# Performance work log

Measured on AMD Instinct MI355X. Metric: run time of the kernel, lower is better.

The kernel has to match this reference:

```python
import jax, jax.numpy as jnp
import numpy as np
from jax import lax

STRIDE = 2
PAD = 2
K = 5

def conv_transpose3d(x, w, b):
    # x: (N, Cin, D, H, W); w: (Cin, Cout, kD, kH, kW) torch layout
    # Equivalent dense conv: flip kernel spatially, swap in/out, lhs-dilate by stride,
    # pad each side by (K - 1 - PAD).
    w_t = jnp.flip(w, axis=(2, 3, 4)).transpose(1, 0, 2, 3, 4)  # (Cout, Cin, kD, kH, kW)
    p = K - 1 - PAD  # = 2
    y = lax.conv_general_dilated(
        x, w_t,
        window_strides=(1, 1, 1),
        padding=[(p, p)] * 3,
        lhs_dilation=(STRIDE,) * 3,
        dimension_numbers=('NCDHW', 'OIDHW', 'NCDHW'))
    return y + b[None, :, None, None, None]

def maxpool3d(x, k):
    return lax.reduce_window(
        x, -jnp.inf, lax.max,
        window_dimensions=(1, 1, k, k, k),
        window_strides=(1, 1, k, k, k),
        padding='VALID')

def setup_inputs() -> dict:
    key = jax.random.key(0)
    k1, k2, k3 = jax.random.split(key, 3)
    x = jax.random.normal(k1, (16, 32, 16, 32, 32), dtype=jnp.float32)
    weight = jax.random.normal(k2, (32, 64, 5, 5, 5), dtype=jnp.float32) * 0.05
    bias = jax.random.normal(k3, (64,), dtype=jnp.float32) * 0.05
    return {"x": x, "weight": weight, "bias": bias}

def reference(x, weight, bias):
    y = conv_transpose3d(x, weight, bias)      # (16, 64, 31, 63, 63)
    y = maxpool3d(y, 2)                        # (16, 64, 15, 31, 31)
    y = maxpool3d(y, 3)                        # (16, 64, 5, 10, 10)
    return jnp.sum(y, axis=1, keepdims=True)   # (16, 1, 5, 10, 10)
```

## Files before the change

kernel.cpp:

```cpp
#include <hip/hip_runtime.h>

typedef short v8s __attribute__((ext_vector_type(8)));
typedef float v4f __attribute__((ext_vector_type(4)));

#define N_  16
#define CI_ 32
#define CO_ 64
#define DI  16
#define HI  32
#define WI  32
#define NEGINF (-__builtin_inff())

__device__ __forceinline__ unsigned short f2bf(float f) {
    unsigned int u = __float_as_uint(f);
    unsigned int r = (u + 0x7FFFu + ((u >> 16) & 1u)) >> 16;
    return (unsigned short)r;
}

__device__ __forceinline__ void gld16(const void* g, void* l) {
    __builtin_amdgcn_global_load_lds(
        (const __attribute__((address_space(1))) void*)g,
        (__attribute__((address_space(3))) void*)l, 16, 0, 0);
}

__constant__ int O64c[9] = {0, 55296, 92160, 129024, 153600, 190464, 215040, 239616, 256000};

__global__ void prep(const float* __restrict__ x, const float* __restrict__ w,
                     unsigned short* __restrict__ xp, unsigned short* __restrict__ wt,
                     float* __restrict__ out, int do_x) {
    if (blockIdx.x < 1088) {
        if (!do_x) return;
        __shared__ __align__(16) unsigned short tl[8192];
        const int bi = blockIdx.x;
        const int pd = bi % 17;
        const int cg = (bi / 17) & 3;
        const int n  = bi / 68;
        if (pd > 0) {
            const int c = threadIdx.x >> 5;
            const int ww = threadIdx.x & 31;
            const float* xc = x + (((size_t)(n * 32 + cg * 8 + c) * 16 + (pd - 1)) * 32) * 32;
            #pragma unroll
            for (int h = 0; h < 32; ++h)
                tl[(h * 32 + ww) * 8 + c] = f2bf(xc[h * 32 + ww]);
        }
        __syncthreads();
        unsigned short* xpo = xp + (size_t)bi * 8448;
        for (int o = threadIdx.x; o < 1056; o += 256) {
            int ph = o / 33, pw = o - ph * 33;
            v8s v;
            if (pd == 0 || ph == 0 || pw == 0) v = (v8s){0, 0, 0, 0, 0, 0, 0, 0};
            else v = *(const v8s*)&tl[((ph - 1) * 32 + pw - 1) * 8];
            *(v8s*)(xpo + o * 8) = v;
        }
    } else {
        if (blockIdx.x == 1088 && threadIdx.x < 64) {
            int tb = 1536 + threadIdx.x;
            int whalf = tb & 1, hj = (tb >> 1) % 10, dj = (tb / 20) % 5, n = tb / 100;
            float* o = out + (((size_t)(n * 5 + dj) * 10 + hj) * 10 + whalf * 5);
            #pragma unroll
            for (int j = 0; j < 5; ++j) o[j] = 0.f;
        }
        int u = (blockIdx.x - 1088) * 256 + threadIdx.x;
        if (u >= 256000) return;
        int r = 0;
        #pragma unroll
        for (int i = 1; i < 8; ++i) r += (u >= O64c[i]);
        const int rd = r >> 2, rh = (r >> 1) & 1, rw = r & 1;
        const int nh = rh ? 2 : 3, nw = rw ? 2 : 3;
        int t2 = u - O64c[r];
        int j   = t2 & 7;
        int l   = (t2 >> 3) & 15;
        int q   = (t2 >> 7) & 3;
        int nt  = (t2 >> 9) & 3;
        int tap = t2 >> 11;
        int co = nt * 16 + l;
        int ci = q * 8 + j;
        int jw = tap % nw;
        int jh = (tap / nw) % nh;
        int jd = tap / (nw * nh);
        int kd = rd + 2 * jd, kh = rh + 2 * jh, kw = rw + 2 * jw;
        wt[u] = f2bf(w[(ci * CO_ + co) * 125 + kd * 25 + kh * 5 + kw]);
    }
}

__device__ __forceinline__ void run_class_rt(
        const unsigned short* __restrict__ xs,
        int laneAB,
        const unsigned short* __restrict__ wcls,
        const int taps, const int nw, const int nh, const bool par,
        unsigned Bm, bool isQ3, float (&pmax)[4][2])
{
    const int R0 = par ? 288 : 0;
    const int R1 = par ? 1440 : 576;
    const int R2 = par ? 2016 : 1728;
    const int R3_ = par ? 3168 : 2880;

    const char* xb = (const char*)xs;

    v4f acc[5][4];
    #pragma unroll
    for (int t = 0; t < 5; ++t)
        #pragma unroll
        for (int nt = 0; nt < 4; ++nt)
            acc[t][nt] = (v4f){0.f, 0.f, 0.f, 0.f};

    v8s B0[4], B1[4];
    #pragma unroll
    for (int nt = 0; nt < 4; ++nt) B0[nt] = *(const v8s*)(wcls + nt * 512);

    int aoff = 0, jw = 0, jh = 0;
    auto adv = [&]() {
        aoff += 16; ++jw;
        if (jw == nw) { jw = 0; aoff += 288 - 16 * nw; ++jh;
            if (jh == nh) { jh = 0; aoff += 1440 - 288 * nh; } }
    };
    auto comp = [&](const v8s (&B)[4]) {
        const int va = laneAB - aoff;
        v8s a0 = *(const v8s*)(xb + va + R0);
        v8s a1 = *(const v8s*)(xb + va + R1);
        v8s a2 = *(const v8s*)(xb + va + R2);
        v8s a3 = *(const v8s*)(xb + va + R3_);
        #pragma unroll
        for (int nt = 0; nt < 4; ++nt) {
            acc[0][nt] = __builtin_amdgcn_mfma_f32_16x16x32_bf16(a0, B[nt], acc[0][nt], 0, 0, 0);
            acc[1][nt] = __builtin_amdgcn_mfma_f32_16x16x32_bf16(a1, B[nt], acc[1][nt], 0, 0, 0);
            acc[2][nt] = __builtin_amdgcn_mfma_f32_16x16x32_bf16(a2, B[nt], acc[2][nt], 0, 0, 0);
            acc[3][nt] = __builtin_amdgcn_mfma_f32_16x16x32_bf16(a3, B[nt], acc[3][nt], 0, 0, 0);
        }
        if (!par) {
            v8s a4 = *(const v8s*)(xb + va + 3456);
            #pragma unroll
            for (int nt = 0; nt < 4; ++nt)
                acc[4][nt] = __builtin_amdgcn_mfma_f32_16x16x32_bf16(a4, B[nt], acc[4][nt], 0, 0, 0);
        }
    };

    int s = 0;
    while (s + 2 <= taps) {
        #pragma unroll
        for (int nt = 0; nt < 4; ++nt)
            B1[nt] = *(const v8s*)(wcls + ((s + 1) * 4 + nt) * 512);
        comp(B0); adv();
        if (s + 2 < taps) {
            #pragma unroll
            for (int nt = 0; nt < 4; ++nt)
                B0[nt] = *(const v8s*)(wcls + ((s + 2) * 4 + nt) * 512);
        }
        comp(B1); adv();
        s += 2;
    }
    if (s < taps) comp(B0);

    #pragma unroll
    for (int nt = 0; nt < 4; ++nt) {
        #pragma unroll
        for (int reg = 0; reg < 4; ++reg) {
            float v = acc[0][nt][reg];
            v = fmaxf(v, acc[1][nt][reg]);
            v = fmaxf(v, acc[2][nt][reg]);
            v = fmaxf(v, acc[3][nt][reg]);
            if (!par) v = fmaxf(v, acc[4][nt][reg]);
            if (reg == 3) v = isQ3 ? NEGINF : v;
            const bool bB = (Bm >> reg) & 1u;
            pmax[nt][0] = fmaxf(pmax[nt][0], bB ? NEGINF : v);
            pmax[nt][1] = fmaxf(pmax[nt][1], bB ? v : NEGINF);
        }
    }
}

__device__ __forceinline__ void run_class_nt1(
        const unsigned short* __restrict__ xs,
        int laneAB,
        const unsigned short* __restrict__ wcls,
        const int taps, const int nw, const int nh, const bool par,
        unsigned Bm, bool isQ3, float (&pmax)[2])
{
    const int R0 = par ? 288 : 0;
    const int R1 = par ? 1440 : 576;
    const int R2 = par ? 2016 : 1728;
    const int R3_ = par ? 3168 : 2880;

    const char* xb = (const char*)xs;

    v4f acc[5];
    #pragma unroll
    for (int t = 0; t < 5; ++t) acc[t] = (v4f){0.f, 0.f, 0.f, 0.f};

    v8s B0 = *(const v8s*)(wcls);
    v8s B1;

    int aoff = 0, jw = 0, jh = 0;
    auto adv = [&]() {
        aoff += 16; ++jw;
        if (jw == nw) { jw = 0; aoff += 288 - 16 * nw; ++jh;
            if (jh == nh) { jh = 0; aoff += 1440 - 288 * nh; } }
    };
    auto comp = [&](v8s B) {
        const int va = laneAB - aoff;
        v8s a0 = *(const v8s*)(xb + va + R0);
        v8s a1 = *(const v8s*)(xb + va + R1);
        v8s a2 = *(const v8s*)(xb + va + R2);
        v8s a3 = *(const v8s*)(xb + va + R3_);
        acc[0] = __builtin_amdgcn_mfma_f32_16x16x32_bf16(a0, B, acc[0], 0, 0, 0);
        acc[1] = __builtin_amdgcn_mfma_f32_16x16x32_bf16(a1, B, acc[1], 0, 0, 0);
        acc[2] = __builtin_amdgcn_mfma_f32_16x16x32_bf16(a2, B, acc[2], 0, 0, 0);
        acc[3] = __builtin_amdgcn_mfma_f32_16x16x32_bf16(a3, B, acc[3], 0, 0, 0);
        if (!par) {
            v8s a4 = *(const v8s*)(xb + va + 3456);
            acc[4] = __builtin_amdgcn_mfma_f32_16x16x32_bf16(a4, B, acc[4], 0, 0, 0);
        }
    };

    int s = 0;
    while (s + 2 <= taps) {
        B1 = *(const v8s*)(wcls + (s + 1) * 2048);
        comp(B0); adv();
        if (s + 2 < taps) B0 = *(const v8s*)(wcls + (s + 2) * 2048);
        comp(B1); adv();
        s += 2;
    }
    if (s < taps) comp(B0);

    #pragma unroll
    for (int reg = 0; reg < 4; ++reg) {
        float v = acc[0][reg];
        v = fmaxf(v, acc[1][reg]);
        v = fmaxf(v, acc[2][reg]);
        v = fmaxf(v, acc[3][reg]);
        if (!par) v = fmaxf(v, acc[4][reg]);
        if (reg == 3) v = isQ3 ? NEGINF : v;
        const bool bB = (Bm >> reg) & 1u;
        pmax[0] = fmaxf(pmax[0], bB ? NEGINF : v);
        pmax[1] = fmaxf(pmax[1], bB ? v : NEGINF);
    }
}

template<bool PRE>
__global__ __launch_bounds__(256, 3)
void fused_main(const float* __restrict__ x, const unsigned short* __restrict__ xp,
                const unsigned short* __restrict__ wt,
                const float* __restrict__ bias, float* __restrict__ out) {
    __shared__ __align__(16) char smem[28800];
    unsigned short* xs = (unsigned short*)smem;
    float* P = (float*)smem;
    float* Y = (float*)(smem + 9472);

    const int b = blockIdx.x;
    const bool tail = (b >= 1536);
    int tile, sub;
    if (tail) { int u = b - 1536; tile = 1536 + (u >> 2); sub = u & 3; }
    else      { tile = b; sub = 0; }

    const int whalf = tile & 1;
    const int hj = (tile >> 1) % 10;
    const int dj = (tile / 20) % 5;
    const int n  = tile / 100;

    const int lane = threadIdx.x & 63;
    const int wv   = threadIdx.x >> 6;

    if (PRE) {
        const int t = threadIdx.x;
        #pragma unroll
        for (int i = 0; i < 8; ++i) {
            int c = i * 256 + t;
            if (c < 1800) {
                int row = c / 18;
                int iwc = c - row * 18;
                int cg  = row / 25;
                int rr  = row - cg * 25;
                int idl = rr / 5;
                int ihl = rr - idl * 5;
                size_t goff = ((((size_t)((n * 4 + cg) * 17 + 3 * dj + idl)) * 32
                                + 3 * hj + ihl) * 33 + 15 * whalf + iwc) * 8;
                gld16(xp + goff, smem + i * 4096 + wv * 1024);
            }
        }
    } else {
        const int id0 = 3 * dj - 1, ih0 = 3 * hj - 1, iwb = 15 * whalf - 1;
        const float* xn = x + (size_t)n * (CI_ * DI * HI * WI);
        for (int e = threadIdx.x; e < 14400; e += 256) {
            int ci   = e / 450;
            int rem  = e - ci * 450;
            int idp  = rem / 90;
            int rem2 = rem - idp * 90;
            int ihp  = rem2 / 18;
            int iwp  = rem2 - ihp * 18;
            int id = id0 + idp, ih = ih0 + ihp, iw = iwb + iwp;
            float v = 0.f;
            if (id >= 0 && ih >= 0 && iw >= 0)
                v = xn[((ci * DI + id) * HI + ih) * WI + iw];
            xs[(ci >> 3) * 3600 + idp * 720 + ihp * 144 + iwp * 8 + (ci & 7)] = f2bf(v);
        }
    }
    __syncthreads();

    const int l = lane & 15, q = lane >> 4;
    const int laneAB = q * 7200 + (l + 2) * 16 + 3456;

    static constexpr int tapsT[8] = {27, 18, 18, 12, 18, 12, 12, 8};
    static constexpr int O64[8]   = {0, 55296, 92160, 129024, 153600, 190464, 215040, 239616};
    static constexpr int nwT[8]   = {3, 2, 3, 2, 3, 2, 3, 2};
    static constexpr int nhT[8]   = {3, 3, 2, 2, 3, 3, 2, 2};
    static constexpr int uOff[5] = {0, 3, 7, 11, 16};
    static constexpr int uR[16] = {0,0,7,  1,2,4,7,  4,1,2,3,  3,5,6,5,6};
    static constexpr int uP[16] = {0,1,0,  0,0,1,1,  0,1,1,1,  0,0,0,1,1};

    static constexpr int wjAt[4] = {0, 1, 2, 4};
    static constexpr int wjBt[4] = {1, 2, 3, 5};

    const unsigned Bm = (0x0EC8u >> (q << 2)) & 0xFu;
    const bool isQ3 = (q == 3);
    const int u0 = uOff[wv], u1 = uOff[wv + 1];

    if (!tail) {
        float pmax[4][2];
        #pragma unroll
        for (int nt = 0; nt < 4; ++nt) { pmax[nt][0] = NEGINF; pmax[nt][1] = NEGINF; }

        #pragma unroll 1
        for (int iu = u0; iu < u1; ++iu) {
            const int  r   = uR[iu];
            const bool par = uP[iu] != 0;
            run_class_rt(xs, laneAB, wt + O64[r] + lane * 8,
                         tapsT[r], nwT[r], nhT[r], par, Bm, isQ3, pmax);
        }

        __syncthreads();
        {
            int base = ((wv * 4 + q) * 16 + l) * 9;
            #pragma unroll
            for (int nt = 0; nt < 4; ++nt) {
                P[base + nt * 2 + 0] = pmax[nt][0];
                P[base + nt * 2 + 1] = pmax[nt][1];
            }
        }
        __syncthreads();

        for (int oi = threadIdx.x; oi < 320; oi += 256) {
            int co = oi / 5;
            int wjl = oi - co * 5;
            int lc = co & 15, ntc = co >> 4;
            float v = NEGINF;
            #pragma unroll
            for (int w = 0; w < 4; ++w) {
                #pragma unroll
                for (int qq = 0; qq < 4; ++qq) {
                    const float* pp = &P[((w * 4 + qq) * 16 + lc) * 9 + ntc * 2];
                    if (wjAt[qq] == wjl) v = fmaxf(v, pp[0]);
                    if (wjBt[qq] == wjl) v = fmaxf(v, pp[1]);
                }
            }
            Y[co * 5 + wjl] = v + bias[co];
        }
        __syncthreads();

        if (wv == 0) {
            float vy[5];
            #pragma unroll
            for (int wjl = 0; wjl < 5; ++wjl) vy[wjl] = Y[lane * 5 + wjl];
            #pragma unroll
            for (int wjl = 0; wjl < 5; ++wjl) {
                float v = vy[wjl];
                #pragma unroll
                for (int off = 32; off > 0; off >>= 1)
                    v += __shfl_down(v, off, 64);
                if (lane == 0)
                    out[((n * 5 + dj) * 10 + hj) * 10 + whalf * 5 + wjl] = v;
            }
        }
    } else {
        float pmax1[2];
        pmax1[0] = NEGINF; pmax1[1] = NEGINF;

        #pragma unroll 1
        for (int iu = u0; iu < u1; ++iu) {
            const int  r   = uR[iu];
            const bool par = uP[iu] != 0;
            run_class_nt1(xs, laneAB, wt + O64[r] + sub * 512 + lane * 8,
                          tapsT[r], nwT[r], nhT[r], par, Bm, isQ3, pmax1);
        }

        __syncthreads();
        {
            int base = ((wv * 4 + q) * 16 + l) * 9;
            P[base + sub * 2 + 0] = pmax1[0];
            P[base + sub * 2 + 1] = pmax1[1];
        }
        __syncthreads();

        if (wv == 0) {
            const int co = lane;
            const int lc = co & 15, ntc = co >> 4;
            const bool valid = (ntc == sub);
            float vy[5];
            #pragma unroll
            for (int wjl = 0; wjl < 5; ++wjl) vy[wjl] = NEGINF;
            #pragma unroll
            for (int w = 0; w < 4; ++w) {
                #pragma unroll
                for (int qq = 0; qq < 4; ++qq) {
                    const float* pp = &P[((w * 4 + qq) * 16 + lc) * 9 + sub * 2];
                    float a = pp[0], bv = pp[1];
                    #pragma unroll
                    for (int wjl = 0; wjl < 5; ++wjl) {
                        if (wjAt[qq] == wjl) vy[wjl] = fmaxf(vy[wjl], a);
                        if (wjBt[qq] == wjl) vy[wjl] = fmaxf(vy[wjl], bv);
                    }
                }
            }
            #pragma unroll
            for (int wjl = 0; wjl < 5; ++wjl) {
                float v = valid ? (vy[wjl] + bias[co]) : 0.f;
                #pragma unroll
                for (int off = 32; off > 0; off >>= 1)
                    v += __shfl_down(v, off, 64);
                if (lane == 0)
                    atomicAdd(&out[((n * 5 + dj) * 10 + hj) * 10 + whalf * 5 + wjl], v);
            }
        }
    }
}

extern "C" void kernel_launch(void* const* d_in, const int* in_sizes, int n_in,
                              void* d_out, int out_size, void* d_ws, size_t ws_size,
                              hipStream_t stream) {
    const float* x    = (const float*)d_in[0];
    const float* w    = (const float*)d_in[1];
    const float* bias = (const float*)d_in[2];
    float*       out  = (float*)d_out;
    unsigned short* wt = (unsigned short*)d_ws;
    unsigned short* xp = (unsigned short*)((char*)d_ws + 512512);
    const size_t XP_NEED = 512512 + 18382848;
    const int do_x = (ws_size >= XP_NEED) ? 1 : 0;

    prep<<<dim3(2088), 256, 0, stream>>>(x, w, xp, wt, out, do_x);
    if (do_x)
        fused_main<true ><<<dim3(1792), 256, 0, stream>>>(x, xp, wt, bias, out);
    else
        fused_main<false><<<dim3(1792), 256, 0, stream>>>(x, xp, wt, bias, out);
}
```

Before: 183.1 us.

## Process all nine row offsets per weight load, rebalance class-to-wave assignment

Each wave now computes all nine output-row groups (both parities) for a parity class in one pass instead of splitting them into separate 4- or 5-row passes. Each loaded weight fragment therefore feeds 36 MFMAs rather than 16 or 20, and weight reloads and loop overhead are removed. The work units are rebalanced to two whole classes per wave. The price is 36 accumulator vectors per lane, so the launch bound drops from 3 to 2 blocks per SM, which lowers occupancy and risks spills.

```diff
diff --git a/kernel.cpp b/kernel.cpp
--- a/kernel.cpp
+++ b/kernel.cpp
@@ -83,23 +83,18 @@
     }
 }
 
-__device__ __forceinline__ void run_class_rt(
+__device__ __forceinline__ void run_class_f(
         const unsigned short* __restrict__ xs,
         int laneAB,
         const unsigned short* __restrict__ wcls,
-        const int taps, const int nw, const int nh, const bool par,
+        const int taps, const int nw, const int nh,
         unsigned Bm, bool isQ3, float (&pmax)[4][2])
 {
-    const int R0 = par ? 288 : 0;
-    const int R1 = par ? 1440 : 576;
-    const int R2 = par ? 2016 : 1728;
-    const int R3_ = par ? 3168 : 2880;
-
     const char* xb = (const char*)xs;
 
-    v4f acc[5][4];
+    v4f acc[9][4];
     #pragma unroll
-    for (int t = 0; t < 5; ++t)
+    for (int t = 0; t < 9; ++t)
         #pragma unroll
         for (int nt = 0; nt < 4; ++nt)
             acc[t][nt] = (v4f){0.f, 0.f, 0.f, 0.f};
@@ -116,22 +111,13 @@
     };
     auto comp = [&](const v8s (&B)[4]) {
         const int va = laneAB - aoff;
-        v8s a0 = *(const v8s*)(xb + va + R0);
-        v8s a1 = *(const v8s*)(xb + va + R1);
-        v8s a2 = *(const v8s*)(xb + va + R2);
-        v8s a3 = *(const v8s*)(xb + va + R3_);
-        #pragma unroll
-        for (int nt = 0; nt < 4; ++nt) {
-            acc[0][nt] = __builtin_amdgcn_mfma_f32_16x16x32_bf16(a0, B[nt], acc[0][nt], 0, 0, 0);
-            acc[1][nt] = __builtin_amdgcn_mfma_f32_16x16x32_bf16(a1, B[nt], acc[1][nt], 0, 0, 0);
-            acc[2][nt] = __builtin_amdgcn_mfma_f32_16x16x32_bf16(a2, B[nt], acc[2][nt], 0, 0, 0);
-            acc[3][nt] = __builtin_amdgcn_mfma_f32_16x16x32_bf16(a3, B[nt], acc[3][nt], 0, 0, 0);
-        }
-        if (!par) {
-            v8s a4 = *(const v8s*)(xb + va + 3456);
+        static constexpr int RO[9] = {0, 576, 1728, 2880, 3456, 288, 1440, 2016, 3168};
+        #pragma unroll
+        for (int rr = 0; rr < 9; ++rr) {
+            v8s a = *(const v8s*)(xb + va + RO[rr]);
             #pragma unroll
             for (int nt = 0; nt < 4; ++nt)
-                acc[4][nt] = __builtin_amdgcn_mfma_f32_16x16x32_bf16(a4, B[nt], acc[4][nt], 0, 0, 0);
+                acc[rr][nt] = __builtin_amdgcn_mfma_f32_16x16x32_bf16(a, B[nt], acc[rr][nt], 0, 0, 0);
         }
     };
 
@@ -156,10 +142,8 @@
         #pragma unroll
         for (int reg = 0; reg < 4; ++reg) {
             float v = acc[0][nt][reg];
-            v = fmaxf(v, acc[1][nt][reg]);
-            v = fmaxf(v, acc[2][nt][reg]);
-            v = fmaxf(v, acc[3][nt][reg]);
-            if (!par) v = fmaxf(v, acc[4][nt][reg]);
+            #pragma unroll
+            for (int rr = 1; rr < 9; ++rr) v = fmaxf(v, acc[rr][nt][reg]);
             if (reg == 3) v = isQ3 ? NEGINF : v;
             const bool bB = (Bm >> reg) & 1u;
             pmax[nt][0] = fmaxf(pmax[nt][0], bB ? NEGINF : v);
@@ -168,23 +152,18 @@
     }
 }
 
-__device__ __forceinline__ void run_class_nt1(
+__device__ __forceinline__ void run_class_t(
         const unsigned short* __restrict__ xs,
         int laneAB,
         const unsigned short* __restrict__ wcls,
-        const int taps, const int nw, const int nh, const bool par,
+        const int taps, const int nw, const int nh,
         unsigned Bm, bool isQ3, float (&pmax)[2])
 {
-    const int R0 = par ? 288 : 0;
-    const int R1 = par ? 1440 : 576;
-    const int R2 = par ? 2016 : 1728;
-    const int R3_ = par ? 3168 : 2880;
-
     const char* xb = (const char*)xs;
 
-    v4f acc[5];
+    v4f acc[9];
     #pragma unroll
-    for (int t = 0; t < 5; ++t) acc[t] = (v4f){0.f, 0.f, 0.f, 0.f};
+    for (int t = 0; t < 9; ++t) acc[t] = (v4f){0.f, 0.f, 0.f, 0.f};
 
     v8s B0 = *(const v8s*)(wcls);
     v8s B1;
@@ -197,17 +176,11 @@
     };
     auto comp = [&](v8s B) {
         const int va = laneAB - aoff;
-        v8s a0 = *(const v8s*)(xb + va + R0);
-        v8s a1 = *(const v8s*)(xb + va + R1);
-        v8s a2 = *(const v8s*)(xb + va + R2);
-        v8s a3 = *(const v8s*)(xb + va + R3_);
-        acc[0] = __builtin_amdgcn_mfma_f32_16x16x32_bf16(a0, B, acc[0], 0, 0, 0);
-        acc[1] = __builtin_amdgcn_mfma_f32_16x16x32_bf16(a1, B, acc[1], 0, 0, 0);
-        acc[2] = __builtin_amdgcn_mfma_f32_16x16x32_bf16(a2, B, acc[2], 0, 0, 0);
-        acc[3] = __builtin_amdgcn_mfma_f32_16x16x32_bf16(a3, B, acc[3], 0, 0, 0);
-        if (!par) {
-            v8s a4 = *(const v8s*)(xb + va + 3456);
-            acc[4] = __builtin_amdgcn_mfma_f32_16x16x32_bf16(a4, B, acc[4], 0, 0, 0);
+        static constexpr int RO[9] = {0, 576, 1728, 2880, 3456, 288, 1440, 2016, 3168};
+        #pragma unroll
+        for (int rr = 0; rr < 9; ++rr) {
+            v8s a = *(const v8s*)(xb + va + RO[rr]);
+            acc[rr] = __builtin_amdgcn_mfma_f32_16x16x32_bf16(a, B, acc[rr], 0, 0, 0);
         }
     };
 
@@ -224,10 +197,8 @@
     #pragma unroll
     for (int reg = 0; reg < 4; ++reg) {
         float v = acc[0][reg];
-        v = fmaxf(v, acc[1][reg]);
-        v = fmaxf(v, acc[2][reg]);
-        v = fmaxf(v, acc[3][reg]);
-        if (!par) v = fmaxf(v, acc[4][reg]);
+        #pragma unroll
+        for (int rr = 1; rr < 9; ++rr) v = fmaxf(v, acc[rr][reg]);
         if (reg == 3) v = isQ3 ? NEGINF : v;
         const bool bB = (Bm >> reg) & 1u;
         pmax[0] = fmaxf(pmax[0], bB ? NEGINF : v);
@@ -236,7 +207,7 @@
 }
 
 template<bool PRE>
-__global__ __launch_bounds__(256, 3)
+__global__ __launch_bounds__(256, 2)
 void fused_main(const float* __restrict__ x, const unsigned short* __restrict__ xp,
                 const unsigned short* __restrict__ wt,
                 const float* __restrict__ bias, float* __restrict__ out) {
@@ -302,9 +273,8 @@
     static constexpr int O64[8]   = {0, 55296, 92160, 129024, 153600, 190464, 215040, 239616};
     static constexpr int nwT[8]   = {3, 2, 3, 2, 3, 2, 3, 2};
     static constexpr int nhT[8]   = {3, 3, 2, 2, 3, 3, 2, 2};
-    static constexpr int uOff[5] = {0, 3, 7, 11, 16};
-    static constexpr int uR[16] = {0,0,7,  1,2,4,7,  4,1,2,3,  3,5,6,5,6};
-    static constexpr int uP[16] = {0,1,0,  0,0,1,1,  0,1,1,1,  0,0,0,1,1};
+    static constexpr int uOff[5] = {0, 2, 4, 6, 8};
+    static constexpr int uR[8]   = {0, 7,  1, 3,  2, 5,  4, 6};
 
     static constexpr int wjAt[4] = {0, 1, 2, 4};
     static constexpr int wjBt[4] = {1, 2, 3, 5};
@@ -320,10 +290,9 @@
 
         #pragma unroll 1
         for (int iu = u0; iu < u1; ++iu) {
-            const int  r   = uR[iu];
-            const bool par = uP[iu] != 0;
-            run_class_rt(xs, laneAB, wt + O64[r] + lane * 8,
-                         tapsT[r], nwT[r], nhT[r], par, Bm, isQ3, pmax);
+            const int r = uR[iu];
+            run_class_f(xs, laneAB, wt + O64[r] + lane * 8,
+                        tapsT[r], nwT[r], nhT[r], Bm, isQ3, pmax);
         }
 
         __syncthreads();
@@ -375,10 +344,9 @@
 
         #pragma unroll 1
         for (int iu = u0; iu < u1; ++iu) {
-            const int  r   = uR[iu];
-            const bool par = uP[iu] != 0;
-            run_class_nt1(xs, laneAB, wt + O64[r] + sub * 512 + lane * 8,
-                          tapsT[r], nwT[r], nhT[r], par, Bm, isQ3, pmax1);
+            const int r = uR[iu];
+            run_class_t(xs, laneAB, wt + O64[r] + sub * 512 + lane * 8,
+                        tapsT[r], nwT[r], nhT[r], Bm, isQ3, pmax1);
         }
 
         __syncthreads();
```

Measured after the change: 174.6 us (median of 2 runs). 1.05x faster.
